# Kernel optimization log

Hardware: AMD Instinct MI355X
Metric: run time of the kernel (lower is better)

The kernel has to match this reference:

```python
import jax, jax.numpy as jnp
import numpy as np

N_HEAD = 16
N_EMBD = 1024
B, T = 4, 1024


def setup_inputs() -> dict:
    key = jax.random.key(0)
    ks = jax.random.split(key, 8)
    hs = N_EMBD // N_HEAD
    x = jax.random.normal(ks[0], (B, T, N_EMBD), dtype=jnp.float32)
    # previous-layer attention load per token, ~O(1/T) like a softmax column mean
    refractory_state = jax.random.uniform(ks[1], (B, T), dtype=jnp.float32) / T
    s_attn = 1.0 / np.sqrt(N_EMBD)
    W_attn = jax.random.normal(ks[2], (N_EMBD, 3 * N_EMBD), dtype=jnp.float32) * s_attn
    b_attn = jnp.zeros((3 * N_EMBD,), dtype=jnp.float32)
    W_proj = jax.random.normal(ks[3], (N_EMBD, N_EMBD), dtype=jnp.float32) * s_attn
    b_proj = jnp.zeros((N_EMBD,), dtype=jnp.float32)
    # learnable LIF params, init per module (lif_mode='refractory')
    threshold = jnp.full((N_HEAD,), 0.01, dtype=jnp.float32)
    leak = jnp.full((N_HEAD,), 2.0, dtype=jnp.float32)
    steepness = jnp.full((N_HEAD,), 2.0, dtype=jnp.float32)
    ref_strength = jnp.full((N_HEAD,), -2.0, dtype=jnp.float32)
    cross_w = jnp.full((N_HEAD,), -2.0, dtype=jnp.float32)
    return {
        "x": x, "refractory_state": refractory_state,
        "W_attn": W_attn, "b_attn": b_attn,
        "W_proj": W_proj, "b_proj": b_proj,
        "threshold": threshold, "leak": leak, "steepness": steepness,
        "ref_strength": ref_strength, "cross_w": cross_w,
    }


def reference(x, refractory_state, W_attn, b_attn, W_proj, b_proj,
              threshold, leak, steepness, ref_strength, cross_w):
    Bq, Tq, C = x.shape
    H = N_HEAD
    hs = C // H
    qkv = x @ W_attn + b_attn                     # [B,T,3C]
    q, k, v = jnp.split(qkv, 3, axis=-1)
    q = q.reshape(Bq, Tq, H, hs).transpose(0, 2, 1, 3)  # [B,H,T,hs]
    k = k.reshape(Bq, Tq, H, hs).transpose(0, 2, 1, 3)
    v = v.reshape(Bq, Tq, H, hs).transpose(0, 2, 1, 3)

    att = jnp.einsum('bhqd,bhkd->bhqk', q, k) * (1.0 / jnp.sqrt(jnp.asarray(hs, x.dtype)))
    causal = jnp.tril(jnp.ones((Tq, Tq), dtype=bool))
    att = jnp.where(causal[None, None], att, -jnp.inf)
    probs = jax.nn.softmax(att, axis=-1)          # [B,H,T,T]

    thr = (jnp.abs(threshold) * 0.1)[None, :, None, None]
    lk = jax.nn.sigmoid(leak)[None, :, None, None]
    st = jax.nn.softplus(steepness)[None, :, None, None]
    # refractory: column load over queries + cross-layer load
    column_load = probs.mean(axis=-2, keepdims=True)          # [B,H,1,T]
    eff_thr = thr + jax.nn.softplus(ref_strength)[None, :, None, None] * column_load
    eff_thr = eff_thr + jax.nn.sigmoid(cross_w)[None, :, None, None] * refractory_state[:, None, None, :]

    fire = jax.nn.sigmoid(st * (probs - eff_thr))
    lif_w = fire + lk * (1.0 - fire)
    mod = probs * lif_w
    mod = mod / (mod.sum(axis=-1, keepdims=True) + 1e-8)
    new_refractory = mod.mean(axis=1).mean(axis=-2)           # [B,T]

    y = jnp.einsum('bhqk,bhkd->bhqd', mod, v)
    y = y.transpose(0, 2, 1, 3).reshape(Bq, Tq, C)
    y = y @ W_proj + b_proj
    return y, new_refractory
```

## Files before the change

kernel.cpp:

```cpp
#include <hip/hip_runtime.h>
#include <math.h>

#define B_  4
#define T_  1024
#define C_  1024
#define H_  16
#define HS_ 64
#define K2E 0.1803368801f
#define LOG2E 1.44269504f

typedef _Float16 f16;
typedef _Float16 f16x8 __attribute__((ext_vector_type(8)));
typedef float f32x4 __attribute__((ext_vector_type(4)));

#define MFMA16(a,b,c) __builtin_amdgcn_mfma_f32_16x16x32_f16(a,b,c,0,0,0)
#define EXP2(x) __builtin_amdgcn_exp2f(x)
#define RCP(x)  __builtin_amdgcn_rcpf(x)

__device__ __forceinline__ void gload16(const f16* g, f16* l){
    __builtin_amdgcn_global_load_lds(
        (const __attribute__((address_space(1))) void*)g,
        (__attribute__((address_space(3))) void*)l, 16, 0, 0);
}

__device__ __forceinline__ float qsum_(float v){
    v += __shfl_xor(v,1,64); v += __shfl_xor(v,2,64);
    v += __shfl_xor(v,4,64); v += __shfl_xor(v,8,64);
    return v;
}
__device__ __forceinline__ float sigmoidf_(float x){ return 1.0f/(1.0f + __expf(-x)); }
__device__ __forceinline__ float softplusf_(float x){ return fmaxf(x, 0.0f) + log1pf(__expf(-fabsf(x))); }

__global__ __launch_bounds__(256) void conv_f16_k(
    const float* __restrict__ in, f16* __restrict__ out, int n8)
{
    int i = blockIdx.x*256 + threadIdx.x;
    if (i < n8){
        const float4* p = (const float4*)in + (size_t)i*2;
        float4 a = p[0], b = p[1];
        f16x8 o;
        o[0]=(f16)a.x; o[1]=(f16)a.y; o[2]=(f16)a.z; o[3]=(f16)a.w;
        o[4]=(f16)b.x; o[5]=(f16)b.y; o[6]=(f16)b.z; o[7]=(f16)b.w;
        *((f16x8*)out + i) = o;
    }
}

__global__ __launch_bounds__(256) void transpose_f16_k(
    const float* __restrict__ in, f16* __restrict__ out, int K, int N)
{
    __shared__ float tl[32][33];
    const int n0 = blockIdx.x*32, k0 = blockIdx.y*32;
    const int c = threadIdx.x & 31, r4 = threadIdx.x >> 5;
    #pragma unroll
    for (int i=0;i<4;i++){
        int r = r4*4 + i;
        tl[r][c] = in[(size_t)(k0+r)*N + n0 + c];
    }
    __syncthreads();
    #pragma unroll
    for (int i=0;i<4;i++){
        int r = r4*4 + i;
        out[(size_t)(n0+r)*K + k0 + c] = (f16)tl[c][r];
    }
}

__global__ __launch_bounds__(256) void gemm_qkv_k(
    const f16* __restrict__ A, const f16* __restrict__ Bt,
    const float* __restrict__ bias,
    f16* __restrict__ Qh, f16* __restrict__ Kh, f16* __restrict__ Vt)
{
    __shared__ __align__(16) f16 Al[8*512];
    __shared__ __align__(16) f16 Bl[8*512];
    const int tid = threadIdx.x;
    const int lane = tid & 63, wave = tid >> 6;
    const int lx = lane & 15, quad = lane >> 4;
    const int wm = wave & 1, wn = wave >> 1;
    const int m0 = blockIdx.y*128, n0 = blockIdx.x*128;
    f32x4 acc[4][4];
    #pragma unroll
    for (int i=0;i<4;i++){
        #pragma unroll
        for (int j=0;j<4;j++){ acc[i][j][0]=0.f;acc[i][j][1]=0.f;acc[i][j][2]=0.f;acc[i][j][3]=0.f; }
    }
    for (int k0=0; k0<1024; k0+=32){
        __syncthreads();
        #pragma unroll
        for (int i=0;i<2;i++){
            int c = i*4 + wave;
            gload16(A  + (size_t)(m0 + c*16 + lx)*1024 + k0 + quad*8, &Al[c*512]);
            gload16(Bt + (size_t)(n0 + c*16 + lx)*1024 + k0 + quad*8, &Bl[c*512]);
        }
        __syncthreads();
        f16x8 af[4], bf[4];
        #pragma unroll
        for (int mt=0;mt<4;mt++) af[mt] = *(const f16x8*)&Al[(wm*4+mt)*512 + quad*128 + lx*8];
        #pragma unroll
        for (int nt=0;nt<4;nt++) bf[nt] = *(const f16x8*)&Bl[(wn*4+nt)*512 + quad*128 + lx*8];
        #pragma unroll
        for (int mt=0;mt<4;mt++){
            #pragma unroll
            for (int nt=0;nt<4;nt++)
                acc[mt][nt] = MFMA16(af[mt], bf[nt], acc[mt][nt]);
        }
    }
    #pragma unroll
    for (int mt=0;mt<4;mt++){
        #pragma unroll
        for (int nt=0;nt<4;nt++){
            int n = n0 + wn*64 + nt*16 + lx;
            int which = n >> 10, cc = n & 1023, h = cc >> 6, d = cc & 63;
            float bv = bias[n];
            #pragma unroll
            for (int r=0;r<4;r++){
                int m = m0 + wm*64 + mt*16 + quad*4 + r;
                int bb = m >> 10, t = m & 1023;
                int bh = bb*16 + h;
                float v = acc[mt][nt][r] + bv;
                if (which==0)      Qh[((size_t)bh*1024 + t)*64 + d] = (f16)v;
                else if (which==1) Kh[((size_t)bh*1024 + t)*64 + d] = (f16)v;
                else               Vt[((size_t)bh*64 + d)*1024 + t] = (f16)v;
            }
        }
    }
}

__global__ __launch_bounds__(256) void gemm_proj_k(
    const f16* __restrict__ A, const f16* __restrict__ Bt,
    const float* __restrict__ bias, float* __restrict__ out)
{
    __shared__ __align__(16) f16 Al[8*512];
    __shared__ __align__(16) f16 Bl[4*512];
    const int tid = threadIdx.x;
    const int lane = tid & 63, wave = tid >> 6;
    const int lx = lane & 15, quad = lane >> 4;
    const int wm = wave & 1, wn = wave >> 1;
    const int m0 = blockIdx.y*128, n0 = blockIdx.x*64;
    f32x4 acc[4][2];
    #pragma unroll
    for (int i=0;i<4;i++){
        #pragma unroll
        for (int j=0;j<2;j++){ acc[i][j][0]=0.f;acc[i][j][1]=0.f;acc[i][j][2]=0.f;acc[i][j][3]=0.f; }
    }
    for (int k0=0; k0<1024; k0+=32){
        __syncthreads();
        #pragma unroll
        for (int i=0;i<3;i++){
            int u = i*4 + wave;
            if (u < 8)
                gload16(A  + (size_t)(m0 + u*16 + lx)*1024 + k0 + quad*8, &Al[u*512]);
            else
                gload16(Bt + (size_t)(n0 + (u-8)*16 + lx)*1024 + k0 + quad*8, &Bl[(u-8)*512]);
        }
        __syncthreads();
        f16x8 af[4], bf[2];
        #pragma unroll
        for (int mt=0;mt<4;mt++) af[mt] = *(const f16x8*)&Al[(wm*4+mt)*512 + quad*128 + lx*8];
        #pragma unroll
        for (int nt=0;nt<2;nt++) bf[nt] = *(const f16x8*)&Bl[(wn*2+nt)*512 + quad*128 + lx*8];
        #pragma unroll
        for (int mt=0;mt<4;mt++){
            #pragma unroll
            for (int nt=0;nt<2;nt++)
                acc[mt][nt] = MFMA16(af[mt], bf[nt], acc[mt][nt]);
        }
    }
    #pragma unroll
    for (int mt=0;mt<4;mt++){
        #pragma unroll
        for (int nt=0;nt<2;nt++){
            int n = n0 + wn*32 + nt*16 + lx;
            float bv = bias[n];
            #pragma unroll
            for (int r=0;r<4;r++){
                int m = m0 + wm*64 + mt*16 + quad*4 + r;
                out[(size_t)m*1024 + n] = acc[mt][nt][r] + bv;
            }
        }
    }
}

__global__ __launch_bounds__(256) void attn_stats_k(
    const f16* __restrict__ Qh, const f16* __restrict__ Kh,
    float* __restrict__ rowl, float* __restrict__ colp)
{
    __shared__ __align__(16) f16 Kl[4096];
    __shared__ float colacc[64];
    const int tid = threadIdx.x;
    const int lane = tid & 63, wave = tid >> 6;
    const int lx = lane & 15, quad = lane >> 4;
    const int g  = 15 - (blockIdx.x >> 6);
    const int bh = blockIdx.x & 63;
    const int qpos = wave*16 + quad*4;

    const size_t qoff = ((size_t)bh*1024 + g*64 + wave*16 + lx)*64;
    f16x8 aq0 = *(const f16x8*)(Qh + qoff + quad*8);
    f16x8 aq1 = *(const f16x8*)(Qh + qoff + 32 + quad*8);

    float ls[4] = {0.f,0.f,0.f,0.f};
    for (int kt=0; kt<=g; kt++){
        __syncthreads();
        #pragma unroll
        for (int i=0;i<2;i++){
            int u = i*4 + wave, c = u & 3, kh = u >> 2;
            gload16(Kh + ((size_t)bh*1024 + kt*64 + c*16 + lx)*64 + kh*32 + quad*8,
                    &Kl[c*1024 + kh*512]);
        }
        __syncthreads();
        const bool diag = (kt == g);
        #pragma unroll
        for (int nt=0;nt<4;nt++){
            f32x4 sc = {0.f,0.f,0.f,0.f};
            f16x8 b0 = *(const f16x8*)&Kl[nt*1024 + quad*128 + lx*8];
            f16x8 b1 = *(const f16x8*)&Kl[nt*1024 + (4+quad)*128 + lx*8];
            sc = MFMA16(aq0, b0, sc);
            sc = MFMA16(aq1, b1, sc);
            #pragma unroll
            for (int r=0;r<4;r++){
                float sv = sc[r];
                if (diag && (nt*16+lx) > (qpos + r)) sv = -1e4f;
                ls[r] += EXP2(sv*K2E);
            }
        }
    }
    float invl[4];
    #pragma unroll
    for (int r=0;r<4;r++){
        float l = qsum_(ls[r]);
        if (lx == 0) rowl[(size_t)bh*1024 + g*64 + qpos + r] = l;
        invl[r] = RCP(l);
    }

    for (int kt=0; kt<=g; kt++){
        __syncthreads();
        #pragma unroll
        for (int i=0;i<2;i++){
            int u = i*4 + wave, c = u & 3, kh = u >> 2;
            gload16(Kh + ((size_t)bh*1024 + kt*64 + c*16 + lx)*64 + kh*32 + quad*8,
                    &Kl[c*1024 + kh*512]);
        }
        if (tid < 64) colacc[tid] = 0.f;
        __syncthreads();
        const bool diag = (kt == g);
        #pragma unroll
        for (int nt=0;nt<4;nt++){
            f32x4 sc = {0.f,0.f,0.f,0.f};
            f16x8 b0 = *(const f16x8*)&Kl[nt*1024 + quad*128 + lx*8];
            f16x8 b1 = *(const f16x8*)&Kl[nt*1024 + (4+quad)*128 + lx*8];
            sc = MFMA16(aq0, b0, sc);
            sc = MFMA16(aq1, b1, sc);
            float csum = 0.f;
            #pragma unroll
            for (int r=0;r<4;r++){
                float sv = sc[r];
                if (diag && (nt*16+lx) > (qpos + r)) sv = -1e4f;
                csum += EXP2(sv*K2E) * invl[r];
            }
            csum += __shfl_xor(csum,16,64); csum += __shfl_xor(csum,32,64);
            if (quad == 0) atomicAdd(&colacc[nt*16+lx], csum);
        }
        __syncthreads();
        if (tid < 64) atomicAdd(&colp[(size_t)bh*1024 + kt*64 + tid], colacc[tid]);
    }
}

__global__ __launch_bounds__(256) void attn_apply_k(
    const f16* __restrict__ Qh, const f16* __restrict__ Kh, const f16* __restrict__ Vt,
    const float* __restrict__ rowl,
    const float* __restrict__ colp, const float* __restrict__ refr,
    const float* __restrict__ threshold, const float* __restrict__ leak,
    const float* __restrict__ steepness, const float* __restrict__ ref_strength,
    const float* __restrict__ cross_w,
    f16* __restrict__ Yh, float* __restrict__ racc)
{
    __shared__ __align__(16) f16 Kl[4096];
    __shared__ __align__(16) f16 Vl[4096];
    __shared__ __align__(16) f16 Pl[4][16*72];
    __shared__ float eb[1024];
    __shared__ float colacc[64];
    const int tid = threadIdx.x;
    const int lane = tid & 63, wave = tid >> 6;
    const int lx = lane & 15, quad = lane >> 4;
    const int g  = 15 - (blockIdx.x >> 6);
    const int bh = blockIdx.x & 63;
    const int b  = bh >> 4, h = bh & 15;
    const int qpos = wave*16 + quad*4;

    const float thr = fabsf(threshold[h])*0.1f;
    const float lk  = sigmoidf_(leak[h]);
    const float st2 = softplusf_(steepness[h]) * LOG2E;
    const float sprT= softplusf_(ref_strength[h]) * (1.0f/T_);
    const float cw  = sigmoidf_(cross_w[h]);
    const float Alk = 1.f - lk;

    {
        float4 cp = *(const float4*)(colp + (size_t)bh*1024 + tid*4);
        float4 rf = *(const float4*)(refr + (size_t)b*1024 + tid*4);
        eb[tid*4+0] = thr + sprT*cp.x + cw*rf.x;
        eb[tid*4+1] = thr + sprT*cp.y + cw*rf.y;
        eb[tid*4+2] = thr + sprT*cp.z + cw*rf.z;
        eb[tid*4+3] = thr + sprT*cp.w + cw*rf.w;
    }

    const size_t qoff = ((size_t)bh*1024 + g*64 + wave*16 + lx)*64;
    f16x8 aq0 = *(const f16x8*)(Qh + qoff + quad*8);
    f16x8 aq1 = *(const f16x8*)(Qh + qoff + 32 + quad*8);

    float invl[4];
    #pragma unroll
    for (int r=0;r<4;r++)
        invl[r] = RCP(rowl[(size_t)bh*1024 + g*64 + qpos + r]);

    f32x4 y[4];
    #pragma unroll
    for (int i=0;i<4;i++){ y[i][0]=0.f;y[i][1]=0.f;y[i][2]=0.f;y[i][3]=0.f; }
    float Dp[4] = {0.f,0.f,0.f,0.f};

    for (int kt=0; kt<=g; kt++){
        __syncthreads();
        #pragma unroll
        for (int i=0;i<4;i++){
            int u = i*4 + wave;
            if (u < 8){
                int c = u & 3, kh = u >> 2;
                gload16(Kh + ((size_t)bh*1024 + kt*64 + c*16 + lx)*64 + kh*32 + quad*8,
                        &Kl[c*1024 + kh*512]);
            } else {
                int v = u - 8, c = v & 3, kh = v >> 2;
                gload16(Vt + ((size_t)bh*64 + c*16 + lx)*1024 + kt*64 + kh*32 + quad*8,
                        &Vl[c*1024 + kh*512]);
            }
        }
        __syncthreads();
        const bool diag = (kt == g);
        #pragma unroll
        for (int nt=0;nt<4;nt++){
            f32x4 sc = {0.f,0.f,0.f,0.f};
            f16x8 b0 = *(const f16x8*)&Kl[nt*1024 + quad*128 + lx*8];
            f16x8 b1 = *(const f16x8*)&Kl[nt*1024 + (4+quad)*128 + lx*8];
            sc = MFMA16(aq0, b0, sc);
            sc = MFMA16(aq1, b1, sc);
            float ec = st2 * eb[kt*64 + nt*16 + lx];
            #pragma unroll
            for (int r=0;r<4;r++){
                float sv = sc[r];
                if (diag && (nt*16+lx) > (qpos + r)) sv = -1e4f;
                float p = EXP2(sv*K2E) * invl[r];
                float e2 = EXP2(ec - st2*p);
                float fire = RCP(1.f + e2);
                float pw = p * (lk + Alk*fire);
                Dp[r] += pw;
                Pl[wave][(quad*4+r)*72 + nt*16 + lx] = (f16)pw;
            }
        }
        f16x8 ap0 = *(const f16x8*)&Pl[wave][lx*72 + quad*8];
        f16x8 ap1 = *(const f16x8*)&Pl[wave][lx*72 + 32 + quad*8];
        #pragma unroll
        for (int dt=0;dt<4;dt++){
            f16x8 bv0 = *(const f16x8*)&Vl[dt*1024 + quad*128 + lx*8];
            f16x8 bv1 = *(const f16x8*)&Vl[dt*1024 + (4+quad)*128 + lx*8];
            y[dt] = MFMA16(ap0, bv0, y[dt]);
            y[dt] = MFMA16(ap1, bv1, y[dt]);
        }
    }
    float invD[4];
    #pragma unroll
    for (int r=0;r<4;r++) invD[r] = RCP(qsum_(Dp[r]) + 1e-8f);
    #pragma unroll
    for (int dt=0;dt<4;dt++){
        #pragma unroll
        for (int r=0;r<4;r++){
            Yh[(size_t)(b*1024 + g*64 + wave*16 + quad*4 + r)*1024 + h*64 + dt*16 + lx]
                = (f16)(y[dt][r]*invD[r]);
        }
    }

    for (int kt=0; kt<=g; kt++){
        __syncthreads();
        #pragma unroll
        for (int i=0;i<2;i++){
            int u = i*4 + wave, c = u & 3, kh = u >> 2;
            gload16(Kh + ((size_t)bh*1024 + kt*64 + c*16 + lx)*64 + kh*32 + quad*8,
                    &Kl[c*1024 + kh*512]);
        }
        if (tid < 64) colacc[tid] = 0.f;
        __syncthreads();
        const bool diag = (kt == g);
        #pragma unroll
        for (int nt=0;nt<4;nt++){
            f32x4 sc = {0.f,0.f,0.f,0.f};
            f16x8 b0 = *(const f16x8*)&Kl[nt*1024 + quad*128 + lx*8];
            f16x8 b1 = *(const f16x8*)&Kl[nt*1024 + (4+quad)*128 + lx*8];
            sc = MFMA16(aq0, b0, sc);
            sc = MFMA16(aq1, b1, sc);
            float ec = st2 * eb[kt*64 + nt*16 + lx];
            float csum = 0.f;
            #pragma unroll
            for (int r=0;r<4;r++){
                float sv = sc[r];
                if (diag && (nt*16+lx) > (qpos + r)) sv = -1e4f;
                float p = EXP2(sv*K2E) * invl[r];
                float e2 = EXP2(ec - st2*p);
                float fire = RCP(1.f + e2);
                csum += p * (lk + Alk*fire) * invD[r];
            }
            csum += __shfl_xor(csum,16,64); csum += __shfl_xor(csum,32,64);
            if (quad == 0) atomicAdd(&colacc[nt*16+lx], csum);
        }
        __syncthreads();
        if (tid < 64) atomicAdd(&racc[(size_t)b*1024 + kt*64 + tid], colacc[tid]);
    }
}

__global__ __launch_bounds__(256) void finish_refr_k(
    const float* __restrict__ racc, float* __restrict__ out)
{
    int i = blockIdx.x*256 + threadIdx.x;
    if (i < B_*T_) out[i] = racc[i] * (1.0f/(H_*T_));
}

extern "C" void kernel_launch(void* const* d_in, const int* in_sizes, int n_in,
                              void* d_out, int out_size, void* d_ws, size_t ws_size,
                              hipStream_t stream) {
    (void)in_sizes; (void)n_in; (void)out_size; (void)ws_size;
    const float* x           = (const float*)d_in[0];
    const float* refr        = (const float*)d_in[1];
    const float* W_attn      = (const float*)d_in[2];
    const float* b_attn      = (const float*)d_in[3];
    const float* W_proj      = (const float*)d_in[4];
    const float* b_proj      = (const float*)d_in[5];
    const float* threshold   = (const float*)d_in[6];
    const float* leak        = (const float*)d_in[7];
    const float* steepness   = (const float*)d_in[8];
    const float* ref_strength= (const float*)d_in[9];
    const float* cross_w     = (const float*)d_in[10];
    float* out = (float*)d_out;

    char* ws = (char*)d_ws;
    f16* x_h = (f16*)ws;                       ws += (size_t)4096*1024*2;
    f16* WaT = (f16*)ws;                       ws += (size_t)3072*1024*2;
    f16* WpT = (f16*)ws;                       ws += (size_t)1024*1024*2;
    f16* Qh  = (f16*)ws;                       ws += (size_t)64*1024*64*2;
    f16* Kh  = (f16*)ws;                       ws += (size_t)64*1024*64*2;
    f16* Vt  = (f16*)ws;                       ws += (size_t)64*64*1024*2;
    f16* Yh  = (f16*)ws;                       ws += (size_t)4096*1024*2;
    float* rowl = (float*)ws;                  ws += (size_t)65536*4;
    float* colp = (float*)ws;                  ws += (size_t)65536*4;
    float* racc = (float*)ws;                  ws += (size_t)4096*4;

    hipMemsetAsync(colp, 0, 65536*sizeof(float), stream);
    hipMemsetAsync(racc, 0, 4096*sizeof(float), stream);

    conv_f16_k<<<dim3(2048), dim3(256), 0, stream>>>(x, x_h, 4096*1024/8);
    transpose_f16_k<<<dim3(96,32), dim3(256), 0, stream>>>(W_attn, WaT, 1024, 3072);
    transpose_f16_k<<<dim3(32,32), dim3(256), 0, stream>>>(W_proj, WpT, 1024, 1024);
    gemm_qkv_k<<<dim3(24,32), dim3(256), 0, stream>>>(x_h, WaT, b_attn, Qh, Kh, Vt);
    attn_stats_k<<<dim3(1024), dim3(256), 0, stream>>>(Qh, Kh, rowl, colp);
    attn_apply_k<<<dim3(1024), dim3(256), 0, stream>>>(
        Qh, Kh, Vt, rowl, colp, refr,
        threshold, leak, steepness, ref_strength, cross_w, Yh, racc);
    gemm_proj_k<<<dim3(16,32), dim3(256), 0, stream>>>(Yh, WpT, b_proj, out);
    finish_refr_k<<<dim3(16), dim3(256), 0, stream>>>(racc, out + (size_t)B_*T_*C_);
}
```

Before: 319.1 us.

## Replace direct global-to-LDS loads with register-prefetched double-staged tile loads

Every GEMM and attention loop now loads the next K/V/A/B tile into registers after the barrier, overlapping it with the current tile's MFMA work. The next iteration then writes those registers to LDS, replacing the synchronous global_load_lds path. This hides global memory latency behind compute, at the cost of extra VGPRs and an explicit LDS write step. The LDS layout written is intended to match the old layout, with index expressions rewritten to an equivalent form.

```diff
diff --git a/kernel.cpp b/kernel.cpp
--- a/kernel.cpp
+++ b/kernel.cpp
@@ -16,12 +16,6 @@
 #define MFMA16(a,b,c) __builtin_amdgcn_mfma_f32_16x16x32_f16(a,b,c,0,0,0)
 #define EXP2(x) __builtin_amdgcn_exp2f(x)
 #define RCP(x)  __builtin_amdgcn_rcpf(x)
-
-__device__ __forceinline__ void gload16(const f16* g, f16* l){
-    __builtin_amdgcn_global_load_lds(
-        (const __attribute__((address_space(1))) void*)g,
-        (__attribute__((address_space(3))) void*)l, 16, 0, 0);
-}
 
 __device__ __forceinline__ float qsum_(float v){
     v += __shfl_xor(v,1,64); v += __shfl_xor(v,2,64);
@@ -82,15 +76,30 @@
         #pragma unroll
         for (int j=0;j<4;j++){ acc[i][j][0]=0.f;acc[i][j][1]=0.f;acc[i][j][2]=0.f;acc[i][j][3]=0.f; }
     }
+    f16x8 ra[2], rb[2];
+    #pragma unroll
+    for (int i=0;i<2;i++){
+        int c = i*4 + wave;
+        ra[i] = *(const f16x8*)(A  + (size_t)(m0 + c*16 + lx)*1024 + quad*8);
+        rb[i] = *(const f16x8*)(Bt + (size_t)(n0 + c*16 + lx)*1024 + quad*8);
+    }
     for (int k0=0; k0<1024; k0+=32){
         __syncthreads();
         #pragma unroll
         for (int i=0;i<2;i++){
             int c = i*4 + wave;
-            gload16(A  + (size_t)(m0 + c*16 + lx)*1024 + k0 + quad*8, &Al[c*512]);
-            gload16(Bt + (size_t)(n0 + c*16 + lx)*1024 + k0 + quad*8, &Bl[c*512]);
-        }
-        __syncthreads();
+            *(f16x8*)&Al[c*512 + quad*128 + lx*8] = ra[i];
+            *(f16x8*)&Bl[c*512 + quad*128 + lx*8] = rb[i];
+        }
+        __syncthreads();
+        if (k0 + 32 < 1024){
+            #pragma unroll
+            for (int i=0;i<2;i++){
+                int c = i*4 + wave;
+                ra[i] = *(const f16x8*)(A  + (size_t)(m0 + c*16 + lx)*1024 + k0+32 + quad*8);
+                rb[i] = *(const f16x8*)(Bt + (size_t)(n0 + c*16 + lx)*1024 + k0+32 + quad*8);
+            }
+        }
         f16x8 af[4], bf[4];
         #pragma unroll
         for (int mt=0;mt<4;mt++) af[mt] = *(const f16x8*)&Al[(wm*4+mt)*512 + quad*128 + lx*8];
@@ -141,17 +150,24 @@
         #pragma unroll
         for (int j=0;j<2;j++){ acc[i][j][0]=0.f;acc[i][j][1]=0.f;acc[i][j][2]=0.f;acc[i][j][3]=0.f; }
     }
+    f16x8 ra[2], rb;
+    #pragma unroll
+    for (int i=0;i<2;i++)
+        ra[i] = *(const f16x8*)(A + (size_t)(m0 + (i*4+wave)*16 + lx)*1024 + quad*8);
+    rb = *(const f16x8*)(Bt + (size_t)(n0 + wave*16 + lx)*1024 + quad*8);
     for (int k0=0; k0<1024; k0+=32){
         __syncthreads();
         #pragma unroll
-        for (int i=0;i<3;i++){
-            int u = i*4 + wave;
-            if (u < 8)
-                gload16(A  + (size_t)(m0 + u*16 + lx)*1024 + k0 + quad*8, &Al[u*512]);
-            else
-                gload16(Bt + (size_t)(n0 + (u-8)*16 + lx)*1024 + k0 + quad*8, &Bl[(u-8)*512]);
-        }
-        __syncthreads();
+        for (int i=0;i<2;i++)
+            *(f16x8*)&Al[(i*4+wave)*512 + quad*128 + lx*8] = ra[i];
+        *(f16x8*)&Bl[wave*512 + quad*128 + lx*8] = rb;
+        __syncthreads();
+        if (k0 + 32 < 1024){
+            #pragma unroll
+            for (int i=0;i<2;i++)
+                ra[i] = *(const f16x8*)(A + (size_t)(m0 + (i*4+wave)*16 + lx)*1024 + k0+32 + quad*8);
+            rb = *(const f16x8*)(Bt + (size_t)(n0 + wave*16 + lx)*1024 + k0+32 + quad*8);
+        }
         f16x8 af[4], bf[2];
         #pragma unroll
         for (int mt=0;mt<4;mt++) af[mt] = *(const f16x8*)&Al[(wm*4+mt)*512 + quad*128 + lx*8];
@@ -191,27 +207,41 @@
     const int g  = 15 - (blockIdx.x >> 6);
     const int bh = blockIdx.x & 63;
     const int qpos = wave*16 + quad*4;
+    const size_t kbase = (size_t)bh*1024*64;
 
     const size_t qoff = ((size_t)bh*1024 + g*64 + wave*16 + lx)*64;
     f16x8 aq0 = *(const f16x8*)(Qh + qoff + quad*8);
     f16x8 aq1 = *(const f16x8*)(Qh + qoff + 32 + quad*8);
 
+    f16x8 rk[2];
+    #pragma unroll
+    for (int i=0;i<2;i++){
+        int u = i*4+wave, c = u&3, kh = u>>2;
+        rk[i] = *(const f16x8*)(Kh + kbase + (size_t)(c*16+lx)*64 + kh*32 + quad*8);
+    }
+
     float ls[4] = {0.f,0.f,0.f,0.f};
     for (int kt=0; kt<=g; kt++){
         __syncthreads();
         #pragma unroll
         for (int i=0;i<2;i++){
-            int u = i*4 + wave, c = u & 3, kh = u >> 2;
-            gload16(Kh + ((size_t)bh*1024 + kt*64 + c*16 + lx)*64 + kh*32 + quad*8,
-                    &Kl[c*1024 + kh*512]);
-        }
-        __syncthreads();
+            int u = i*4+wave, c = u&3, kh = u>>2;
+            *(f16x8*)&Kl[c*1024 + kh*512 + quad*128 + lx*8] = rk[i];
+        }
+        __syncthreads();
+        if (kt < g){
+            #pragma unroll
+            for (int i=0;i<2;i++){
+                int u = i*4+wave, c = u&3, kh = u>>2;
+                rk[i] = *(const f16x8*)(Kh + kbase + (size_t)((kt+1)*64 + c*16+lx)*64 + kh*32 + quad*8);
+            }
+        }
         const bool diag = (kt == g);
         #pragma unroll
         for (int nt=0;nt<4;nt++){
             f32x4 sc = {0.f,0.f,0.f,0.f};
             f16x8 b0 = *(const f16x8*)&Kl[nt*1024 + quad*128 + lx*8];
-            f16x8 b1 = *(const f16x8*)&Kl[nt*1024 + (4+quad)*128 + lx*8];
+            f16x8 b1 = *(const f16x8*)&Kl[nt*1024 + 512 + quad*128 + lx*8];
             sc = MFMA16(aq0, b0, sc);
             sc = MFMA16(aq1, b1, sc);
             #pragma unroll
@@ -230,22 +260,33 @@
         invl[r] = RCP(l);
     }
 
+    #pragma unroll
+    for (int i=0;i<2;i++){
+        int u = i*4+wave, c = u&3, kh = u>>2;
+        rk[i] = *(const f16x8*)(Kh + kbase + (size_t)(c*16+lx)*64 + kh*32 + quad*8);
+    }
     for (int kt=0; kt<=g; kt++){
         __syncthreads();
         #pragma unroll
         for (int i=0;i<2;i++){
-            int u = i*4 + wave, c = u & 3, kh = u >> 2;
-            gload16(Kh + ((size_t)bh*1024 + kt*64 + c*16 + lx)*64 + kh*32 + quad*8,
-                    &Kl[c*1024 + kh*512]);
+            int u = i*4+wave, c = u&3, kh = u>>2;
+            *(f16x8*)&Kl[c*1024 + kh*512 + quad*128 + lx*8] = rk[i];
         }
         if (tid < 64) colacc[tid] = 0.f;
         __syncthreads();
+        if (kt < g){
+            #pragma unroll
+            for (int i=0;i<2;i++){
+                int u = i*4+wave, c = u&3, kh = u>>2;
+                rk[i] = *(const f16x8*)(Kh + kbase + (size_t)((kt+1)*64 + c*16+lx)*64 + kh*32 + quad*8);
+            }
+        }
         const bool diag = (kt == g);
         #pragma unroll
         for (int nt=0;nt<4;nt++){
             f32x4 sc = {0.f,0.f,0.f,0.f};
             f16x8 b0 = *(const f16x8*)&Kl[nt*1024 + quad*128 + lx*8];
-            f16x8 b1 = *(const f16x8*)&Kl[nt*1024 + (4+quad)*128 + lx*8];
+            f16x8 b1 = *(const f16x8*)&Kl[nt*1024 + 512 + quad*128 + lx*8];
             sc = MFMA16(aq0, b0, sc);
             sc = MFMA16(aq1, b1, sc);
             float csum = 0.f;
@@ -284,6 +325,7 @@
     const int bh = blockIdx.x & 63;
     const int b  = bh >> 4, h = bh & 15;
     const int qpos = wave*16 + quad*4;
+    const size_t kbase = (size_t)bh*1024*64;
 
     const float thr = fabsf(threshold[h])*0.1f;
     const float lk  = sigmoidf_(leak[h]);
@@ -315,28 +357,37 @@
     for (int i=0;i<4;i++){ y[i][0]=0.f;y[i][1]=0.f;y[i][2]=0.f;y[i][3]=0.f; }
     float Dp[4] = {0.f,0.f,0.f,0.f};
 
+    f16x8 rk[2], rv[2];
+    #pragma unroll
+    for (int i=0;i<2;i++){
+        int u = i*4+wave, c = u&3, kh = u>>2;
+        rk[i] = *(const f16x8*)(Kh + kbase + (size_t)(c*16+lx)*64 + kh*32 + quad*8);
+        rv[i] = *(const f16x8*)(Vt + kbase + (size_t)(c*16+lx)*1024 + kh*32 + quad*8);
+    }
+
     for (int kt=0; kt<=g; kt++){
         __syncthreads();
         #pragma unroll
-        for (int i=0;i<4;i++){
-            int u = i*4 + wave;
-            if (u < 8){
-                int c = u & 3, kh = u >> 2;
-                gload16(Kh + ((size_t)bh*1024 + kt*64 + c*16 + lx)*64 + kh*32 + quad*8,
-                        &Kl[c*1024 + kh*512]);
-            } else {
-                int v = u - 8, c = v & 3, kh = v >> 2;
-                gload16(Vt + ((size_t)bh*64 + c*16 + lx)*1024 + kt*64 + kh*32 + quad*8,
-                        &Vl[c*1024 + kh*512]);
-            }
-        }
-        __syncthreads();
+        for (int i=0;i<2;i++){
+            int u = i*4+wave, c = u&3, kh = u>>2;
+            *(f16x8*)&Kl[c*1024 + kh*512 + quad*128 + lx*8] = rk[i];
+            *(f16x8*)&Vl[c*1024 + kh*512 + quad*128 + lx*8] = rv[i];
+        }
+        __syncthreads();
+        if (kt < g){
+            #pragma unroll
+            for (int i=0;i<2;i++){
+                int u = i*4+wave, c = u&3, kh = u>>2;
+                rk[i] = *(const f16x8*)(Kh + kbase + (size_t)((kt+1)*64 + c*16+lx)*64 + kh*32 + quad*8);
+                rv[i] = *(const f16x8*)(Vt + kbase + (size_t)(c*16+lx)*1024 + (kt+1)*64 + kh*32 + quad*8);
+            }
+        }
         const bool diag = (kt == g);
         #pragma unroll
         for (int nt=0;nt<4;nt++){
             f32x4 sc = {0.f,0.f,0.f,0.f};
             f16x8 b0 = *(const f16x8*)&Kl[nt*1024 + quad*128 + lx*8];
-            f16x8 b1 = *(const f16x8*)&Kl[nt*1024 + (4+quad)*128 + lx*8];
+            f16x8 b1 = *(const f16x8*)&Kl[nt*1024 + 512 + quad*128 + lx*8];
             sc = MFMA16(aq0, b0, sc);
             sc = MFMA16(aq1, b1, sc);
             float ec = st2 * eb[kt*64 + nt*16 + lx];
@@ -357,7 +408,7 @@
         #pragma unroll
         for (int dt=0;dt<4;dt++){
             f16x8 bv0 = *(const f16x8*)&Vl[dt*1024 + quad*128 + lx*8];
-            f16x8 bv1 = *(const f16x8*)&Vl[dt*1024 + (4+quad)*128 + lx*8];
+            f16x8 bv1 = *(const f16x8*)&Vl[dt*1024 + 512 + quad*128 + lx*8];
             y[dt] = MFMA16(ap0, bv0, y[dt]);
             y[dt] = MFMA16(ap1, bv1, y[dt]);
         }
@@ -374,22 +425,33 @@
         }
     }
 
+    #pragma unroll
+    for (int i=0;i<2;i++){
+        int u = i*4+wave, c = u&3, kh = u>>2;
+        rk[i] = *(const f16x8*)(Kh + kbase + (size_t)(c*16+lx)*64 + kh*32 + quad*8);
+    }
     for (int kt=0; kt<=g; kt++){
         __syncthreads();
         #pragma unroll
         for (int i=0;i<2;i++){
-            int u = i*4 + wave, c = u & 3, kh = u >> 2;
-            gload16(Kh + ((size_t)bh*1024 + kt*64 + c*16 + lx)*64 + kh*32 + quad*8,
-                    &Kl[c*1024 + kh*512]);
+            int u = i*4+wave, c = u&3, kh = u>>2;
+            *(f16x8*)&Kl[c*1024 + kh*512 + quad*128 + lx*8] = rk[i];
         }
         if (tid < 64) colacc[tid] = 0.f;
         __syncthreads();
+        if (kt < g){
+            #pragma unroll
+            for (int i=0;i<2;i++){
+                int u = i*4+wave, c = u&3, kh = u>>2;
+                rk[i] = *(const f16x8*)(Kh + kbase + (size_t)((kt+1)*64 + c*16+lx)*64 + kh*32 + quad*8);
+            }
+        }
         const bool diag = (kt == g);
         #pragma unroll
         for (int nt=0;nt<4;nt++){
             f32x4 sc = {0.f,0.f,0.f,0.f};
             f16x8 b0 = *(const f16x8*)&Kl[nt*1024 + quad*128 + lx*8];
-            f16x8 b1 = *(const f16x8*)&Kl[nt*1024 + (4+quad)*128 + lx*8];
+            f16x8 b1 = *(const f16x8*)&Kl[nt*1024 + 512 + quad*128 + lx*8];
             sc = MFMA16(aq0, b0, sc);
             sc = MFMA16(aq1, b1, sc);
             float ec = st2 * eb[kt*64 + nt*16 + lx];
```

Result: faster. 302.8 us (-5.1%).
